# Optimization experiments

Hardware: AMD Instinct MI355X
Metric: run time of the kernel (lower is better)

Reference implementation:

```python
import jax, jax.numpy as jnp
import numpy as np

B, T, C, H = 2, 2048, 2048, 16
D = C // H  # head_dim = 128
SCALE = 1.0 / np.sqrt(D)


def setup_inputs() -> dict:
    key = jax.random.key(0)
    ks = jax.random.split(key, 9)
    x = jax.random.normal(ks[0], (B, T, C), dtype=jnp.float32)
    # additive causal mask [T, T]
    attn_mask = jnp.where(jnp.tril(jnp.ones((T, T), dtype=bool)), 0.0, -1e9).astype(jnp.float32)
    s_cc = 1.0 / np.sqrt(C)
    s_cd = 1.0 / np.sqrt(C)
    Wq = jax.random.normal(ks[1], (C, C), dtype=jnp.float32) * s_cc
    Wk = jax.random.normal(ks[2], (D, C), dtype=jnp.float32) * s_cd
    Wv = jax.random.normal(ks[3], (D, C), dtype=jnp.float32) * s_cd
    Wo = jax.random.normal(ks[4], (C, C), dtype=jnp.float32) * s_cc
    bq = jnp.zeros((C,), jnp.float32)
    bk = jnp.zeros((D,), jnp.float32)
    bv = jnp.zeros((D,), jnp.float32)
    bo = jnp.zeros((C,), jnp.float32)
    return {"x": x, "attn_mask": attn_mask, "Wq": Wq, "bq": bq, "Wk": Wk,
            "bk": bk, "Wv": Wv, "bv": bv, "Wo": Wo, "bo": bo}


def reference(x, attn_mask, Wq, bq, Wk, bk, Wv, bv, Wo, bo):
    # projections (torch Linear: x @ W.T + b)
    q = (x @ Wq.T + bq).reshape(B, T, H, D).transpose(0, 2, 1, 3)  # [B,H,T,D]
    k = x @ Wk.T + bk                                              # [B,T,D] single KV head
    v = x @ Wv.T + bv                                              # [B,T,D]
    # scores: broadcast shared K over all H query heads
    scores = jnp.einsum('bhtd,bsd->bhts', q, k) * SCALE            # [B,H,T,T]
    scores = scores + attn_mask  # [T,T] broadcasts over B,H
    attn = jax.nn.softmax(scores, axis=-1)
    out = jnp.einsum('bhts,bsd->bhtd', attn, v)                    # [B,H,T,D]
    out = out.transpose(0, 2, 1, 3).reshape(B, T, C)
    return out @ Wo.T + bo
```

## Files before the change

kernel.cpp:

```cpp
#include <hip/hip_runtime.h>
#include <stdint.h>

typedef unsigned short u16;
typedef __attribute__((ext_vector_type(8))) __bf16 bf16x8;
typedef __attribute__((ext_vector_type(4))) float f32x4;
typedef __attribute__((ext_vector_type(8))) u16 u16x8;

#define B_SZ 2
#define T_SZ 2048
#define C_SZ 2048
#define H_SZ 16
#define D_SZ 128
#define NQKV 2304
#define ATT_SCALE 0.08838834764831845f
#define LOG2E_SCALE 0.12751744f
#define DEFER_THR 90.50967f

typedef __attribute__((address_space(1))) void* as1_void_p;
typedef __attribute__((address_space(3))) void* as3_void_p;

__device__ __forceinline__ u16 f2b(float f) {
  union { float f; uint32_t u; } c; c.f = f;
  return (u16)((c.u + 0x7FFFu + ((c.u >> 16) & 1u)) >> 16);
}

__device__ __forceinline__ void gload_lds16(const u16* g, u16* l) {
  __builtin_amdgcn_global_load_lds((as1_void_p)g, (as3_void_p)l, 16, 0, 0);
}

__global__ __launch_bounds__(256) void cast_to_bf16(const float* __restrict__ in,
                                                    u16* __restrict__ out, int n) {
  int idx = (blockIdx.x * 256 + threadIdx.x) * 4;
  if (idx >= n) return;
  float4 f = *(const float4*)&in[idx];
  ushort4 o4;
  o4.x = f2b(f.x); o4.y = f2b(f.y); o4.z = f2b(f.z); o4.w = f2b(f.w);
  *(ushort4*)&out[idx] = o4;
}

__global__ __launch_bounds__(256) void build_bias(const float* __restrict__ bq,
                                                  const float* __restrict__ bk,
                                                  const float* __restrict__ bv,
                                                  float* __restrict__ out) {
  int i = blockIdx.x * 256 + threadIdx.x;
  if (i < C_SZ) out[i] = bq[i];
  else if (i < C_SZ + D_SZ) out[i] = bk[i - C_SZ];
  else if (i < NQKV) out[i] = bv[i - C_SZ - D_SZ];
}

template <typename OutT>
__global__ __launch_bounds__(256) void gemm_bt(const u16* __restrict__ A,
                                               const u16* __restrict__ Bm,
                                               const float* __restrict__ bias,
                                               OutT* __restrict__ C,
                                               int K, int ldc) {
  __shared__ u16 lsA[2][128 * 32];
  __shared__ u16 lsB[2][128 * 32];
  const int tid = threadIdx.x;
  const int lane = tid & 63;
  const int wave = tid >> 6;
  const int wr = wave >> 1, wc = wave & 1;
  const int l16 = lane & 15, lq = lane >> 4;
  const int brow = blockIdx.y * 128;
  const int bcol = blockIdx.x * 128;

  f32x4 acc[4][4] = {};

  auto STAGE = [&](int k0, int bs) {
#pragma unroll
    for (int i = 0; i < 2; i++) {
      const int woff = (i * 4 + wave) * 512;
      const int eoff = woff + lane * 8;
      const int r = eoff >> 5, c = eoff & 31;
      gload_lds16(A + (size_t)(brow + r) * K + k0 + c, &lsA[bs][woff]);
      gload_lds16(Bm + (size_t)(bcol + r) * K + k0 + c, &lsB[bs][woff]);
    }
  };

  STAGE(0, 0);
  __syncthreads();
  int cur = 0;
  for (int k0 = 0; k0 < K; k0 += 32) {
    if (k0 + 32 < K) STAGE(k0 + 32, cur ^ 1);

    bf16x8 af[4], bfr[4];
#pragma unroll
    for (int mi = 0; mi < 4; mi++)
      af[mi] = *(const bf16x8*)&lsA[cur][(wr * 64 + mi * 16 + l16) * 32 + lq * 8];
#pragma unroll
    for (int ni = 0; ni < 4; ni++)
      bfr[ni] = *(const bf16x8*)&lsB[cur][(wc * 64 + ni * 16 + l16) * 32 + lq * 8];
#pragma unroll
    for (int mi = 0; mi < 4; mi++)
#pragma unroll
      for (int ni = 0; ni < 4; ni++)
        acc[mi][ni] = __builtin_amdgcn_mfma_f32_16x16x32_bf16(af[mi], bfr[ni], acc[mi][ni], 0, 0, 0);

    __syncthreads();
    cur ^= 1;
  }

#pragma unroll
  for (int mi = 0; mi < 4; mi++)
#pragma unroll
    for (int ni = 0; ni < 4; ni++) {
      const int col = bcol + wc * 64 + ni * 16 + l16;
      const float bb = bias ? bias[col] : 0.0f;
#pragma unroll
      for (int r = 0; r < 4; r++) {
        const int row = brow + wr * 64 + mi * 16 + lq * 4 + r;
        const float v = acc[mi][ni][r] + bb;
        if constexpr (sizeof(OutT) == 2) {
          ((u16*)C)[(size_t)row * ldc + col] = f2b(v);
        } else {
          ((float*)C)[(size_t)row * ldc + col] = v;
        }
      }
    }
}

__global__ __launch_bounds__(256) void transpose_v(const u16* __restrict__ qkv,
                                                   u16* __restrict__ vT) {
  __shared__ u16 tile[64 * 136];
  const int tid = threadIdx.x;
  const int t0 = blockIdx.x * 64;
  const int b = blockIdx.y;
#pragma unroll
  for (int i = 0; i < 4; i++) {
    int idx = (i * 256 + tid) * 8;
    int r = idx >> 7, c = idx & 127;
    u16x8 v = *(const u16x8*)&qkv[(size_t)(b * T_SZ + t0 + r) * NQKV + (C_SZ + D_SZ) + c];
    *(u16x8*)&tile[r * 136 + c] = v;
  }
  __syncthreads();
#pragma unroll
  for (int i = 0; i < 4; i++) {
    int idx = (i * 256 + tid) * 8;
    int d = idx >> 6, t = idx & 63;
    u16x8 v;
#pragma unroll
    for (int j = 0; j < 8; j++) v[j] = tile[(t + j) * 136 + d];
    *(u16x8*)&vT[(size_t)(b * D_SZ + d) * T_SZ + t0 + t] = v;
  }
}

template <bool MASK>
__device__ __forceinline__ void attn_tile64(
    const u16* lk, const u16* lv, u16* lsPw,
    const bf16x8 (&aq)[4], f32x4 (&o)[8], float (&lp)[4], float& mgrp,
    int relq, int l16, int lq)
{
  f32x4 s[4] = {};
#pragma unroll
  for (int kk = 0; kk < 4; kk++) {
#pragma unroll
    for (int nb = 0; nb < 4; nb++) {
      const int row = nb * 16 + l16;
      const bf16x8 bk = *(const bf16x8*)&lk[row * 128 + (((kk * 4 + lq) ^ (row & 7)) << 3)];
      s[nb] = __builtin_amdgcn_mfma_f32_16x16x32_bf16(aq[kk], bk, s[nb], 0, 0, 0);
    }
  }
  if (MASK) {
#pragma unroll
    for (int nb = 0; nb < 4; nb++)
#pragma unroll
      for (int rr = 0; rr < 4; rr++)
        if (nb * 16 + l16 > relq + rr) s[nb][rr] -= 1e9f;
  }
  float mx = s[0][0];
#pragma unroll
  for (int nb = 0; nb < 4; nb++)
#pragma unroll
    for (int rr = 0; rr < 4; rr++) mx = fmaxf(mx, s[nb][rr]);
#pragma unroll
  for (int sh = 8; sh >= 1; sh >>= 1) mx = fmaxf(mx, __shfl_xor(mx, sh, 64));
  if (__any(mx > mgrp + DEFER_THR)) {
    const float mnew = fmaxf(mgrp, mx);
    const float alpha = exp2f((mgrp - mnew) * LOG2E_SCALE);
    mgrp = mnew;
#pragma unroll
    for (int rr = 0; rr < 4; rr++) lp[rr] *= alpha;
#pragma unroll
    for (int nd = 0; nd < 8; nd++)
#pragma unroll
      for (int e = 0; e < 4; e++) o[nd][e] *= alpha;
  }
#pragma unroll
  for (int nb = 0; nb < 4; nb++)
#pragma unroll
    for (int rr = 0; rr < 4; rr++) {
      const float p = exp2f((s[nb][rr] - mgrp) * LOG2E_SCALE);
      lp[rr] += p;
      const int qr = lq * 4 + rr;
      const int col = nb * 16 + l16;
      lsPw[qr * 64 + ((((col >> 3) ^ (qr & 7)) << 3) | (col & 7))] = f2b(p);
    }
  asm volatile("s_waitcnt lgkmcnt(0)" ::: "memory");
  __builtin_amdgcn_sched_barrier(0);
#pragma unroll
  for (int ks = 0; ks < 2; ks++) {
    const bf16x8 pa = *(const bf16x8*)&lsPw[l16 * 64 + (((ks * 4 + lq) ^ (l16 & 7)) << 3)];
#pragma unroll
    for (int nd = 0; nd < 8; nd++) {
      const int row = nd * 16 + l16;
      const bf16x8 bv = *(const bf16x8*)&lv[row * 64 + (((ks * 4 + lq) ^ (row & 7)) << 3)];
      o[nd] = __builtin_amdgcn_mfma_f32_16x16x32_bf16(pa, bv, o[nd], 0, 0, 0);
    }
  }
}

__global__ __launch_bounds__(256, 2) void attn_fwd(const u16* __restrict__ qkv,
                                                   const u16* __restrict__ vT,
                                                   u16* __restrict__ out) {
  __shared__ u16 lsK[2][64 * 128];
  __shared__ u16 lsV[2][128 * 64];
  __shared__ u16 lsP[4][16 * 64];
  const int tid = threadIdx.x;
  const int w = tid >> 6, lane = tid & 63;
  const int l16 = lane & 15, lq = lane >> 4;
  const int qL = blockIdx.x;
  const int qH = 31 - qL;
  const int h = blockIdx.y;
  const int b = blockIdx.z;
  const int bT = b * T_SZ;

  bf16x8 aqL[4], aqH[4];
  {
    const size_t rL = (size_t)(bT + qL * 64 + w * 16 + l16) * NQKV + h * D_SZ;
    const size_t rH = (size_t)(bT + qH * 64 + w * 16 + l16) * NQKV + h * D_SZ;
#pragma unroll
    for (int kk = 0; kk < 4; kk++) {
      aqL[kk] = *(const bf16x8*)&qkv[rL + kk * 32 + lq * 8];
      aqH[kk] = *(const bf16x8*)&qkv[rH + kk * 32 + lq * 8];
    }
  }

  f32x4 oL[8] = {}, oH[8] = {};
  float lpL[4] = {0.f, 0.f, 0.f, 0.f};
  float lpH[4] = {0.f, 0.f, 0.f, 0.f};
  float mL = -INFINITY, mH = -INFINITY;
  const int relDiag = w * 16 + lq * 4;

  auto STAGE = [&](int kt, int bufsel) {
    const int kv0 = kt << 6;
#pragma unroll
    for (int j = 0; j < 4; j++) {
      const int idx = w * 256 + j * 64 + lane;
      const int row = idx >> 4, c = idx & 15;
      const int sc = c ^ (row & 7);
      gload_lds16(qkv + (size_t)(bT + kv0 + row) * NQKV + C_SZ + sc * 8,
                  &lsK[bufsel][w * 2048 + j * 512]);
    }
#pragma unroll
    for (int j = 0; j < 4; j++) {
      const int idx = w * 256 + j * 64 + lane;
      const int row = idx >> 3, c = idx & 7;
      const int sc = c ^ (row & 7);
      gload_lds16(vT + (size_t)(b * D_SZ + row) * T_SZ + kv0 + sc * 8,
                  &lsV[bufsel][w * 2048 + j * 512]);
    }
  };

  STAGE(0, 0);
  __syncthreads();
  int cur = 0;
  for (int kt = 0; kt <= qH; kt++) {
    if (kt < qH) STAGE(kt + 1, cur ^ 1);
    if (kt == qH)
      attn_tile64<true>(lsK[cur], lsV[cur], lsP[w], aqH, oH, lpH, mH, relDiag, l16, lq);
    else
      attn_tile64<false>(lsK[cur], lsV[cur], lsP[w], aqH, oH, lpH, mH, 0, l16, lq);
    if (kt == qL)
      attn_tile64<true>(lsK[cur], lsV[cur], lsP[w], aqL, oL, lpL, mL, relDiag, l16, lq);
    else if (kt < qL)
      attn_tile64<false>(lsK[cur], lsV[cur], lsP[w], aqL, oL, lpL, mL, 0, l16, lq);
    __syncthreads();
    cur ^= 1;
  }

  float rL4[4], rH4[4];
#pragma unroll
  for (int rr = 0; rr < 4; rr++) {
    float a = lpL[rr], c = lpH[rr];
#pragma unroll
    for (int sh = 8; sh >= 1; sh >>= 1) {
      a += __shfl_xor(a, sh, 64);
      c += __shfl_xor(c, sh, 64);
    }
    rL4[rr] = __builtin_amdgcn_rcpf(a);
    rH4[rr] = __builtin_amdgcn_rcpf(c);
  }
#pragma unroll
  for (int nd = 0; nd < 8; nd++)
#pragma unroll
    for (int rr = 0; rr < 4; rr++) {
      const int rL_ = qL * 64 + w * 16 + lq * 4 + rr;
      const int rH_ = qH * 64 + w * 16 + lq * 4 + rr;
      out[(size_t)(bT + rL_) * C_SZ + h * D_SZ + nd * 16 + l16] = f2b(oL[nd][rr] * rL4[rr]);
      out[(size_t)(bT + rH_) * C_SZ + h * D_SZ + nd * 16 + l16] = f2b(oH[nd][rr] * rH4[rr]);
    }
}

extern "C" void kernel_launch(void* const* d_in, const int* in_sizes, int n_in,
                              void* d_out, int out_size, void* d_ws, size_t ws_size,
                              hipStream_t stream) {
  const float* x  = (const float*)d_in[0];
  const float* Wq = (const float*)d_in[2];
  const float* bq = (const float*)d_in[3];
  const float* Wk = (const float*)d_in[4];
  const float* bk = (const float*)d_in[5];
  const float* Wv = (const float*)d_in[6];
  const float* bv = (const float*)d_in[7];
  const float* Wo = (const float*)d_in[8];
  const float* bo = (const float*)d_in[9];
  float* out = (float*)d_out;

  char* ws = (char*)d_ws;
  if (ws_size < 71312384) return;
  u16* xb     = (u16*)(ws + 0);
  u16* wqkv   = (u16*)(ws + 16777216);
  u16* wob    = (u16*)(ws + 26214400);
  u16* qkv    = (u16*)(ws + 34603008);
  u16* vT     = (u16*)(ws + 53477376);
  u16* ao     = (u16*)(ws + 54525952);
  float* bqkv = (float*)(ws + 71303168);

  cast_to_bf16<<<8192, 256, 0, stream>>>(x, xb, 8388608);
  cast_to_bf16<<<4096, 256, 0, stream>>>(Wq, wqkv, 4194304);
  cast_to_bf16<<<256, 256, 0, stream>>>(Wk, wqkv + 4194304, 262144);
  cast_to_bf16<<<256, 256, 0, stream>>>(Wv, wqkv + 4456448, 262144);
  cast_to_bf16<<<4096, 256, 0, stream>>>(Wo, wob, 4194304);
  build_bias<<<9, 256, 0, stream>>>(bq, bk, bv, bqkv);

  gemm_bt<u16><<<dim3(18, 32), 256, 0, stream>>>(xb, wqkv, bqkv, qkv, 2048, NQKV);
  transpose_v<<<dim3(32, 2), 256, 0, stream>>>(qkv, vT);
  attn_fwd<<<dim3(16, 16, 2), 256, 0, stream>>>(qkv, vT, ao);
  gemm_bt<float><<<dim3(16, 32), 256, 0, stream>>>(ao, wob, bo, out, 2048, 2048);
}
```

Measured before the change: 225.1 us.

## Keep attention probabilities in registers via transposed S=K·Q^T MFMA layout

Swaps the MFMA operand order so each lane holds a column of scores for one query, letting the probabilities feed the PV MFMA (16x16x16) directly from registers instead of round-tripping through LDS. This removes the per-wave P LDS buffer, the waitcnt and sched barrier, and narrows the row-max and row-sum reductions to two cross-lane shuffles. It also precomputes staging pointers and vectorizes the output stores. The trade-off is twice as many smaller MFMAs for the PV product and more complex V fragment indexing.

```diff
diff --git a/kernel.cpp b/kernel.cpp
--- a/kernel.cpp
+++ b/kernel.cpp
@@ -3,8 +3,11 @@
 
 typedef unsigned short u16;
 typedef __attribute__((ext_vector_type(8))) __bf16 bf16x8;
+typedef __attribute__((ext_vector_type(4))) __bf16 bf16x4;
 typedef __attribute__((ext_vector_type(4))) float f32x4;
 typedef __attribute__((ext_vector_type(8))) u16 u16x8;
+typedef __attribute__((ext_vector_type(4))) short s16x4;
+typedef __attribute__((ext_vector_type(2))) unsigned int u32x2;
 
 #define B_SZ 2
 #define T_SZ 2048
@@ -26,6 +29,21 @@
 
 __device__ __forceinline__ void gload_lds16(const u16* g, u16* l) {
   __builtin_amdgcn_global_load_lds((as1_void_p)g, (as3_void_p)l, 16, 0, 0);
+}
+
+__device__ __forceinline__ f32x4 mfma16(s16x4 a, s16x4 b, f32x4 c) {
+#if __has_builtin(__builtin_amdgcn_mfma_f32_16x16x16bf16_1k)
+  return __builtin_amdgcn_mfma_f32_16x16x16bf16_1k(a, b, c, 0, 0, 0);
+#elif __has_builtin(__builtin_amdgcn_mfma_f32_16x16x16_bf16)
+  return __builtin_amdgcn_mfma_f32_16x16x16_bf16(
+      __builtin_bit_cast(bf16x4, a), __builtin_bit_cast(bf16x4, b), c, 0, 0, 0);
+#else
+  u32x2 ua = __builtin_bit_cast(u32x2, a);
+  u32x2 ub = __builtin_bit_cast(u32x2, b);
+  asm("s_nop 1\n\tv_mfma_f32_16x16x16_bf16 %0, %1, %2, %0\n\ts_nop 7"
+      : "+v"(c) : "v"(ua), "v"(ub));
+  return c;
+#endif
 }
 
 __global__ __launch_bounds__(256) void cast_to_bf16(const float* __restrict__ in,
@@ -146,9 +164,9 @@
 
 template <bool MASK>
 __device__ __forceinline__ void attn_tile64(
-    const u16* lk, const u16* lv, u16* lsPw,
-    const bf16x8 (&aq)[4], f32x4 (&o)[8], float (&lp)[4], float& mgrp,
-    int relq, int l16, int lq)
+    const u16* lk, const u16* lv,
+    const bf16x8 (&aq)[4], f32x4 (&o)[8], float& lp, float& m,
+    int q_rel, int l16, int lq)
 {
   f32x4 s[4] = {};
 #pragma unroll
@@ -156,8 +174,8 @@
 #pragma unroll
     for (int nb = 0; nb < 4; nb++) {
       const int row = nb * 16 + l16;
-      const bf16x8 bk = *(const bf16x8*)&lk[row * 128 + (((kk * 4 + lq) ^ (row & 7)) << 3)];
-      s[nb] = __builtin_amdgcn_mfma_f32_16x16x32_bf16(aq[kk], bk, s[nb], 0, 0, 0);
+      const bf16x8 kf = *(const bf16x8*)&lk[row * 128 + (((kk * 4 + lq) ^ (row & 7)) << 3)];
+      s[nb] = __builtin_amdgcn_mfma_f32_16x16x32_bf16(kf, aq[kk], s[nb], 0, 0, 0);
     }
   }
   if (MASK) {
@@ -165,46 +183,40 @@
     for (int nb = 0; nb < 4; nb++)
 #pragma unroll
       for (int rr = 0; rr < 4; rr++)
-        if (nb * 16 + l16 > relq + rr) s[nb][rr] -= 1e9f;
+        if (nb * 16 + lq * 4 + rr > q_rel) s[nb][rr] -= 1e9f;
   }
   float mx = s[0][0];
 #pragma unroll
   for (int nb = 0; nb < 4; nb++)
 #pragma unroll
     for (int rr = 0; rr < 4; rr++) mx = fmaxf(mx, s[nb][rr]);
-#pragma unroll
-  for (int sh = 8; sh >= 1; sh >>= 1) mx = fmaxf(mx, __shfl_xor(mx, sh, 64));
-  if (__any(mx > mgrp + DEFER_THR)) {
-    const float mnew = fmaxf(mgrp, mx);
-    const float alpha = exp2f((mgrp - mnew) * LOG2E_SCALE);
-    mgrp = mnew;
-#pragma unroll
-    for (int rr = 0; rr < 4; rr++) lp[rr] *= alpha;
+  mx = fmaxf(mx, __shfl_xor(mx, 16, 64));
+  mx = fmaxf(mx, __shfl_xor(mx, 32, 64));
+  if (__any(mx > m + DEFER_THR)) {
+    const float mnew = fmaxf(m, mx);
+    const float alpha = exp2f((m - mnew) * LOG2E_SCALE);
+    m = mnew;
+    lp *= alpha;
 #pragma unroll
     for (int nd = 0; nd < 8; nd++)
 #pragma unroll
       for (int e = 0; e < 4; e++) o[nd][e] *= alpha;
   }
 #pragma unroll
-  for (int nb = 0; nb < 4; nb++)
-#pragma unroll
-    for (int rr = 0; rr < 4; rr++) {
-      const float p = exp2f((s[nb][rr] - mgrp) * LOG2E_SCALE);
-      lp[rr] += p;
-      const int qr = lq * 4 + rr;
-      const int col = nb * 16 + l16;
-      lsPw[qr * 64 + ((((col >> 3) ^ (qr & 7)) << 3) | (col & 7))] = f2b(p);
-    }
-  asm volatile("s_waitcnt lgkmcnt(0)" ::: "memory");
-  __builtin_amdgcn_sched_barrier(0);
-#pragma unroll
-  for (int ks = 0; ks < 2; ks++) {
-    const bf16x8 pa = *(const bf16x8*)&lsPw[l16 * 64 + (((ks * 4 + lq) ^ (l16 & 7)) << 3)];
+  for (int nb = 0; nb < 4; nb++) {
+    s16x4 pb;
+#pragma unroll
+    for (int e = 0; e < 4; e++) {
+      const float p = exp2f((s[nb][e] - m) * LOG2E_SCALE);
+      lp += p;
+      pb[e] = (short)f2b(p);
+    }
 #pragma unroll
     for (int nd = 0; nd < 8; nd++) {
       const int row = nd * 16 + l16;
-      const bf16x8 bv = *(const bf16x8*)&lv[row * 64 + (((ks * 4 + lq) ^ (row & 7)) << 3)];
-      o[nd] = __builtin_amdgcn_mfma_f32_16x16x32_bf16(pa, bv, o[nd], 0, 0, 0);
+      const s16x4 av = *(const s16x4*)&lv[row * 64 +
+          ((((nb << 1) | (lq >> 1)) ^ (row & 7)) << 3) + ((lq & 1) << 2)];
+      o[nd] = mfma16(av, pb, o[nd]);
     }
   }
 }
@@ -214,7 +226,6 @@
                                                    u16* __restrict__ out) {
   __shared__ u16 lsK[2][64 * 128];
   __shared__ u16 lsV[2][128 * 64];
-  __shared__ u16 lsP[4][16 * 64];
   const int tid = threadIdx.x;
   const int w = tid >> 6, lane = tid & 63;
   const int l16 = lane & 15, lq = lane >> 4;
@@ -236,28 +247,29 @@
   }
 
   f32x4 oL[8] = {}, oH[8] = {};
-  float lpL[4] = {0.f, 0.f, 0.f, 0.f};
-  float lpH[4] = {0.f, 0.f, 0.f, 0.f};
+  float lpL = 0.f, lpH = 0.f;
   float mL = -INFINITY, mH = -INFINITY;
-  const int relDiag = w * 16 + lq * 4;
+  const int relDiag = w * 16 + l16;
+
+  const u16* kp[4];
+  const u16* vp[4];
+#pragma unroll
+  for (int j = 0; j < 4; j++) {
+    const int rk = w * 16 + j * 4 + (lane >> 4);
+    const int ck = (lane & 15) ^ (rk & 7);
+    kp[j] = qkv + (size_t)(bT + rk) * NQKV + C_SZ + ck * 8;
+    const int rv = w * 32 + j * 8 + (lane >> 3);
+    const int cv = (lane & 7) ^ (rv & 7);
+    vp[j] = vT + (size_t)(b * D_SZ + rv) * T_SZ + cv * 8;
+  }
 
   auto STAGE = [&](int kt, int bufsel) {
-    const int kv0 = kt << 6;
+    const size_t koff = (size_t)kt * (64 * NQKV);
+    const int voff = kt * 64;
 #pragma unroll
     for (int j = 0; j < 4; j++) {
-      const int idx = w * 256 + j * 64 + lane;
-      const int row = idx >> 4, c = idx & 15;
-      const int sc = c ^ (row & 7);
-      gload_lds16(qkv + (size_t)(bT + kv0 + row) * NQKV + C_SZ + sc * 8,
-                  &lsK[bufsel][w * 2048 + j * 512]);
-    }
-#pragma unroll
-    for (int j = 0; j < 4; j++) {
-      const int idx = w * 256 + j * 64 + lane;
-      const int row = idx >> 3, c = idx & 7;
-      const int sc = c ^ (row & 7);
-      gload_lds16(vT + (size_t)(b * D_SZ + row) * T_SZ + kv0 + sc * 8,
-                  &lsV[bufsel][w * 2048 + j * 512]);
+      gload_lds16(kp[j] + koff, &lsK[bufsel][w * 2048 + j * 512]);
+      gload_lds16(vp[j] + voff, &lsV[bufsel][w * 2048 + j * 512]);
     }
   };
 
@@ -267,38 +279,33 @@
   for (int kt = 0; kt <= qH; kt++) {
     if (kt < qH) STAGE(kt + 1, cur ^ 1);
     if (kt == qH)
-      attn_tile64<true>(lsK[cur], lsV[cur], lsP[w], aqH, oH, lpH, mH, relDiag, l16, lq);
+      attn_tile64<true>(lsK[cur], lsV[cur], aqH, oH, lpH, mH, relDiag, l16, lq);
     else
-      attn_tile64<false>(lsK[cur], lsV[cur], lsP[w], aqH, oH, lpH, mH, 0, l16, lq);
+      attn_tile64<false>(lsK[cur], lsV[cur], aqH, oH, lpH, mH, 0, l16, lq);
     if (kt == qL)
-      attn_tile64<true>(lsK[cur], lsV[cur], lsP[w], aqL, oL, lpL, mL, relDiag, l16, lq);
+      attn_tile64<true>(lsK[cur], lsV[cur], aqL, oL, lpL, mL, relDiag, l16, lq);
     else if (kt < qL)
-      attn_tile64<false>(lsK[cur], lsV[cur], lsP[w], aqL, oL, lpL, mL, 0, l16, lq);
+      attn_tile64<false>(lsK[cur], lsV[cur], aqL, oL, lpL, mL, 0, l16, lq);
     __syncthreads();
     cur ^= 1;
   }
 
-  float rL4[4], rH4[4];
-#pragma unroll
-  for (int rr = 0; rr < 4; rr++) {
-    float a = lpL[rr], c = lpH[rr];
-#pragma unroll
-    for (int sh = 8; sh >= 1; sh >>= 1) {
-      a += __shfl_xor(a, sh, 64);
-      c += __shfl_xor(c, sh, 64);
-    }
-    rL4[rr] = __builtin_amdgcn_rcpf(a);
-    rH4[rr] = __builtin_amdgcn_rcpf(c);
-  }
-#pragma unroll
-  for (int nd = 0; nd < 8; nd++)
-#pragma unroll
-    for (int rr = 0; rr < 4; rr++) {
-      const int rL_ = qL * 64 + w * 16 + lq * 4 + rr;
-      const int rH_ = qH * 64 + w * 16 + lq * 4 + rr;
-      out[(size_t)(bT + rL_) * C_SZ + h * D_SZ + nd * 16 + l16] = f2b(oL[nd][rr] * rL4[rr]);
-      out[(size_t)(bT + rH_) * C_SZ + h * D_SZ + nd * 16 + l16] = f2b(oH[nd][rr] * rH4[rr]);
-    }
+  lpL += __shfl_xor(lpL, 16, 64); lpL += __shfl_xor(lpL, 32, 64);
+  lpH += __shfl_xor(lpH, 16, 64); lpH += __shfl_xor(lpH, 32, 64);
+  const float rL = __builtin_amdgcn_rcpf(lpL);
+  const float rH = __builtin_amdgcn_rcpf(lpH);
+  const size_t rowL = (size_t)(bT + qL * 64 + w * 16 + l16) * C_SZ + h * D_SZ;
+  const size_t rowH = (size_t)(bT + qH * 64 + w * 16 + l16) * C_SZ + h * D_SZ;
+#pragma unroll
+  for (int nd = 0; nd < 8; nd++) {
+    ushort4 sL, sH;
+    sL.x = f2b(oL[nd][0] * rL); sL.y = f2b(oL[nd][1] * rL);
+    sL.z = f2b(oL[nd][2] * rL); sL.w = f2b(oL[nd][3] * rL);
+    sH.x = f2b(oH[nd][0] * rH); sH.y = f2b(oH[nd][1] * rH);
+    sH.z = f2b(oH[nd][2] * rH); sH.w = f2b(oH[nd][3] * rH);
+    *(ushort4*)&out[rowL + nd * 16 + lq * 4] = sL;
+    *(ushort4*)&out[rowH + nd * 16 + lq * 4] = sH;
+  }
 }
 
 extern "C" void kernel_launch(void* const* d_in, const int* in_sizes, int n_in,
```

After: 228.0 us. About the same (+1.3%).
